# Kernel tuning notes

Hardware: AMD Instinct MI355X
Metric: run time of the kernel (lower is better)

## Reference

```python
import jax, jax.numpy as jnp
import numpy as np

NEG_SLOPE = 0.2


def gat_conv(x, src, dst, W, a_src, a_dst, bias, heads, out_ch):
    # x: [N, F_in]; src/dst: [E] (message flows src -> dst, softmax over dst)
    N = x.shape[0]
    h = (x @ W).reshape(N, heads, out_ch)              # [N, H, C]
    alpha_s = (h * a_src).sum(-1)                      # [N, H]
    alpha_d = (h * a_dst).sum(-1)                      # [N, H]
    e = jax.nn.leaky_relu(alpha_s[src] + alpha_d[dst], NEG_SLOPE)  # [E, H]
    # segment softmax over destination nodes (every node has a self loop)
    emax = jax.ops.segment_max(e, dst, num_segments=N)             # [N, H]
    ee = jnp.exp(e - emax[dst])
    denom = jax.ops.segment_sum(ee, dst, num_segments=N)           # [N, H]
    alpha = ee / denom[dst]                                        # [E, H]
    msg = h[src] * alpha[..., None]                                # [E, H, C]
    out = jax.ops.segment_sum(msg, dst, num_segments=N)            # [N, H, C]
    return out.reshape(N, heads * out_ch) + bias


def setup_inputs() -> dict:
    key = jax.random.key(0)
    ks = jax.random.split(key, 12)
    N, E, EL = 100000, 1600000, 100000
    F_in, C, H = 128, 64, 2
    glorot = lambda k, shp: jax.random.normal(k, shp, jnp.float32) * np.sqrt(2.0 / (shp[0] + shp[-1]))
    return {
        "x": jax.random.normal(ks[0], (N, F_in), jnp.float32),
        "edge_index": jax.random.randint(ks[1], (2, E), 0, N, jnp.int32),
        "edge_label_index": jax.random.randint(ks[2], (2, EL), 0, N, jnp.int32),
        "W1": glorot(ks[3], (F_in, H * C)),
        "a_src1": glorot(ks[4], (H, C)),
        "a_dst1": glorot(ks[5], (H, C)),
        "b1": jnp.zeros((H * C,), jnp.float32),
        "W2": glorot(ks[6], (H * C, C)),
        "a_src2": glorot(ks[7], (1, C)),
        "a_dst2": glorot(ks[8], (1, C)),
        "b2": jnp.zeros((C,), jnp.float32),
    }


def reference(x, edge_index, edge_label_index, W1, a_src1, a_dst1, b1, W2, a_src2, a_dst2, b2):
    N = x.shape[0]
    # add self loops (PyG GATConv default)
    loop = jnp.arange(N, dtype=edge_index.dtype)
    src = jnp.concatenate([edge_index[0], loop])
    dst = jnp.concatenate([edge_index[1], loop])
    H, C = a_src1.shape[0], a_src1.shape[1]
    z = jax.nn.elu(gat_conv(x, src, dst, W1, a_src1, a_dst1, b1, H, C))
    z = gat_conv(z, src, dst, W2, a_src2, a_dst2, b2, 1, C)         # [N, C]
    # decode: dot product of endpoint embeddings
    return (z[edge_label_index[0]] * z[edge_label_index[1]]).sum(axis=1)
```

## Files before the change

kernel.cpp:

```cpp
#include <hip/hip_runtime.h>
#include <hip/hip_bf16.h>

#define NEG_SLOPE 0.2f
#define LRELU(v) ((v) > 0.f ? (v) : NEG_SLOPE * (v))
#define BBITS 7
#define BSZ 128
#define BCAP 3072

typedef unsigned short ushort_t;
typedef unsigned int uint_t;
typedef float v2f __attribute__((ext_vector_type(2)));
typedef float f32x4 __attribute__((ext_vector_type(4)));
typedef short bf16x8 __attribute__((ext_vector_type(8)));

static inline int cdiv(int a, int b) { return (a + b - 1) / b; }

__device__ __forceinline__ float wsum(float v) {
#pragma unroll
    for (int o = 32; o; o >>= 1) v += __shfl_xor(v, o);
    return v;
}
__device__ __forceinline__ ushort_t f2bfbits(float f) {
    __hip_bfloat16 b = __float2bfloat16(f);
    return *reinterpret_cast<ushort_t*>(&b);
}

__global__ __launch_bounds__(256) void k_zero_int(int* p, int n) {
    int i = blockIdx.x * 256 + threadIdx.x;
    if (i < n) p[i] = 0;
}

__global__ __launch_bounds__(256) void k_bscatter(const int* __restrict__ ei, int E, int ET, int NB,
                                                  int* __restrict__ bcur,
                                                  uint_t* __restrict__ tmp) {
    extern __shared__ int sm2[];
    int* hist = sm2;
    int* cur = sm2 + NB;
    const int CH = 8192;
    int c0 = blockIdx.x * CH;
    int c1 = min(ET, c0 + CH);
    for (int i = threadIdx.x; i < NB; i += 256) hist[i] = 0;
    __syncthreads();
    for (int i = c0 + threadIdx.x; i < c1; i += 256) {
        int d = (i < E) ? ei[E + i] : (i - E);
        atomicAdd(&hist[d >> BBITS], 1);
    }
    __syncthreads();
    for (int i = threadIdx.x; i < NB; i += 256) {
        int c = hist[i];
        cur[i] = c ? atomicAdd(&bcur[i], c) : 0;
    }
    __syncthreads();
    for (int i = c0 + threadIdx.x; i < c1; i += 256) {
        int s = (i < E) ? ei[i] : (i - E);
        int d = (i < E) ? ei[E + i] : (i - E);
        int b = d >> BBITS;
        int pos = atomicAdd(&cur[b], 1);
        pos = min(pos, BCAP - 1);
        tmp[(size_t)b * BCAP + pos] = ((uint_t)(d & (BSZ - 1)) << 25) | (uint_t)s;
    }
}

__global__ void k_scan_small(const int* __restrict__ bcnt, int NB,
                             int* __restrict__ boff, int* __restrict__ offs, int N, int ET) {
    extern __shared__ int sm[];
    for (int i = threadIdx.x; i < NB; i += blockDim.x) sm[i] = bcnt[i];
    __syncthreads();
    if (threadIdx.x == 0) {
        int run = 0;
        for (int i = 0; i < NB; i++) { int c = sm[i]; sm[i] = run; run += c; }
    }
    __syncthreads();
    for (int i = threadIdx.x; i < NB; i += blockDim.x) boff[i] = sm[i];
    if (threadIdx.x == 0) { boff[NB] = ET; offs[N] = ET; }
}

__global__ __launch_bounds__(256) void k_csrfin(const uint_t* __restrict__ tmp,
                                                const int* __restrict__ boff, int NB, int N,
                                                int* __restrict__ offs, int* __restrict__ ssrc) {
    __shared__ int deg[BSZ], cur[BSZ], sc[BSZ];
    int b = blockIdx.x;
    int node0 = b << BBITS;
    int nn = min(BSZ, N - node0);
    int r0 = boff[b], r1 = boff[b + 1];
    int cnt = r1 - r0;
    const uint_t* tb = tmp + (size_t)b * BCAP;
    int t = threadIdx.x;
    if (t < BSZ) deg[t] = 0;
    __syncthreads();
    for (int j = t; j < cnt; j += 256) {
        int dloc = (int)(tb[j] >> 25);
        atomicAdd(&deg[dloc], 1);
    }
    __syncthreads();
    if (t < BSZ) sc[t] = deg[t];
    __syncthreads();
    for (int o = 1; o < BSZ; o <<= 1) {
        int v = 0;
        if (t < BSZ && t >= o) v = sc[t - o];
        __syncthreads();
        if (t < BSZ) sc[t] += v;
        __syncthreads();
    }
    if (t < BSZ) {
        int ex = sc[t] - deg[t];
        cur[t] = r0 + ex;
        if (t < nn) offs[node0 + t] = r0 + ex;
    }
    __syncthreads();
    for (int j = t; j < cnt; j += 256) {
        uint_t v = tb[j];
        int dloc = (int)(v >> 25);
        int s = (int)(v & 0x1FFFFFFu);
        int pos = atomicAdd(&cur[dloc], 1);
        ssrc[pos] = s;
    }
}

__global__ __launch_bounds__(256) void k_wt(const float* __restrict__ W1, ushort_t* __restrict__ Wt1,
                                            const float* __restrict__ W2, ushort_t* __restrict__ Wt2) {
    int idx = blockIdx.x * 256 + threadIdx.x;
    if (idx < 128 * 128) {
        int k = idx >> 7, n = idx & 127;
        Wt1[n * 128 + k] = f2bfbits(W1[idx]);
    } else if (idx < 128 * 128 + 128 * 64) {
        int j = idx - 128 * 128;
        int k = j >> 6, n = j & 63;
        Wt2[n * 128 + k] = f2bfbits(W2[j]);
    }
}

template <int M, int H, bool INBF16>
__global__ __launch_bounds__(256) void k_gemm_mfma(const void* __restrict__ xin,
                                                   const ushort_t* __restrict__ Wt,
                                                   const float* __restrict__ a_src,
                                                   const float* __restrict__ a_dst,
                                                   ushort_t* __restrict__ h,
                                                   float* __restrict__ as, float* __restrict__ ad,
                                                   int N) {
    constexpr int T = M / 16;
    int t = threadIdx.x;
    int w = t >> 6;
    int lane = t & 63;
    int ln = lane & 15;
    int q = lane >> 4;
    int rowA = blockIdx.x * 64 + w * 16 + ln;
    int rowD0 = blockIdx.x * 64 + w * 16 + q * 4;

    f32x4 acc[T];
#pragma unroll
    for (int i = 0; i < T; i++) acc[i] = (f32x4){0.f, 0.f, 0.f, 0.f};

#pragma unroll
    for (int kc = 0; kc < 4; kc++) {
        bf16x8 afrag;
        if (INBF16) {
            if (rowA < N)
                afrag = *(const bf16x8*)((const ushort_t*)xin + (size_t)rowA * 128 + kc * 32 + q * 8);
            else
#pragma unroll
                for (int j = 0; j < 8; j++) afrag[j] = 0;
        } else {
            float xv[8];
            if (rowA < N) {
                const float* xf = (const float*)xin;
                float4 v0 = *(const float4*)(xf + (size_t)rowA * 128 + kc * 32 + q * 8);
                float4 v1 = *(const float4*)(xf + (size_t)rowA * 128 + kc * 32 + q * 8 + 4);
                xv[0] = v0.x; xv[1] = v0.y; xv[2] = v0.z; xv[3] = v0.w;
                xv[4] = v1.x; xv[5] = v1.y; xv[6] = v1.z; xv[7] = v1.w;
            } else {
#pragma unroll
                for (int j = 0; j < 8; j++) xv[j] = 0.f;
            }
#pragma unroll
            for (int j = 0; j < 8; j++) afrag[j] = (short)f2bfbits(xv[j]);
        }
#pragma unroll
        for (int tt = 0; tt < T; tt++) {
            bf16x8 bfrag = *(const bf16x8*)(Wt + (size_t)(tt * 16 + ln) * 128 + kc * 32 + q * 8);
            acc[tt] = __builtin_amdgcn_mfma_f32_16x16x32_bf16(afrag, bfrag, acc[tt], 0, 0, 0);
        }
    }

#pragma unroll
    for (int tt = 0; tt < T; tt++)
#pragma unroll
        for (int r = 0; r < 4; r++) {
            int row = rowD0 + r;
            if (row < N) h[(size_t)row * M + tt * 16 + ln] = f2bfbits(acc[tt][r]);
        }

    float avs[T], avd[T];
#pragma unroll
    for (int tt = 0; tt < T; tt++) {
        avs[tt] = a_src[tt * 16 + ln];
        avd[tt] = a_dst[tt * 16 + ln];
    }
#pragma unroll
    for (int r = 0; r < 4; r++) {
        int row = rowD0 + r;
        if (H == 2) {
            float ps0 = 0.f, ps1 = 0.f, pd0 = 0.f, pd1 = 0.f;
#pragma unroll
            for (int tt = 0; tt < T / 2; tt++) { ps0 += acc[tt][r] * avs[tt]; pd0 += acc[tt][r] * avd[tt]; }
#pragma unroll
            for (int tt = T / 2; tt < T; tt++) { ps1 += acc[tt][r] * avs[tt]; pd1 += acc[tt][r] * avd[tt]; }
#pragma unroll
            for (int o = 8; o; o >>= 1) {
                ps0 += __shfl_down(ps0, o, 16); pd0 += __shfl_down(pd0, o, 16);
                ps1 += __shfl_down(ps1, o, 16); pd1 += __shfl_down(pd1, o, 16);
            }
            if (ln == 0 && row < N) {
                as[(size_t)row * 2] = ps0; as[(size_t)row * 2 + 1] = ps1;
                ad[(size_t)row * 2] = pd0; ad[(size_t)row * 2 + 1] = pd1;
            }
        } else {
            float ps = 0.f, pd = 0.f;
#pragma unroll
            for (int tt = 0; tt < T; tt++) { ps += acc[tt][r] * avs[tt]; pd += acc[tt][r] * avd[tt]; }
#pragma unroll
            for (int o = 8; o; o >>= 1) {
                ps += __shfl_down(ps, o, 16); pd += __shfl_down(pd, o, 16);
            }
            if (ln == 0 && row < N) { as[row] = ps; ad[row] = pd; }
        }
    }
}

template <int H, bool ELU_ACT, bool OUT_BF16>
__global__ __launch_bounds__(256) void k_agg_fused(const int* __restrict__ offs,
                                                   const int* __restrict__ ssrc,
                                                   const float* __restrict__ as,
                                                   const float* __restrict__ ad,
                                                   const ushort_t* __restrict__ h,
                                                   const float* __restrict__ bias,
                                                   void* __restrict__ z, int N) {
    constexpr int G = 16 * H;
    constexpr int EPW = 64 / G;
    constexpr int RB = H * 128;
    __shared__ __align__(16) uint2 lmeta[4][64 * H];
    int wv = threadIdx.x >> 6;
    int lane = threadIdx.x & 63;
    int d = (blockIdx.x * 256 + threadIdx.x) >> 6;
    if (d >= N) return;
    uint2* mw = lmeta[wv];
    int cpos = lane % G;
    int sub = lane / G;
    int hself = (H == 2) ? (cpos >> 4) : 0;
    const char* hb = (const char*)h;
    int cpo8 = cpos * 8;
    const char* mbase = (const char*)mw + ((H == 2) ? (sub * 16 + hself * 8) : (sub * 8));

    float adh0 = ad[(size_t)d * H];
    float adh1 = (H == 2) ? ad[(size_t)d * H + 1] : 0.f;
    float denp[2] = {0.f, 0.f};
    v2f acc2[2];
    acc2[0] = (v2f){0.f, 0.f};
    acc2[1] = (v2f){0.f, 0.f};

    int e0 = offs[d], e1 = offs[d + 1];
    for (int cb = e0; cb < e1; cb += 64) {
        int ne = min(64, e1 - cb);
        unsigned so = 0;
        float p0 = 0.f, p1 = 0.f;
        if (lane < ne) {
            int s_l = ssrc[cb + lane];
            so = (unsigned)s_l * RB;
            if (H == 2) {
                float2 av = ((const float2*)as)[s_l];
                p0 = __expf(LRELU(av.x + adh0));
                p1 = __expf(LRELU(av.y + adh1));
            } else {
                p0 = __expf(LRELU(as[s_l] + adh0));
            }
        }
        denp[0] += p0;
        denp[1] += p1;
        if (H == 2) {
            ((uint4*)mw)[lane] = make_uint4(so, __float_as_uint(p0), so, __float_as_uint(p1));
        } else {
            mw[lane] = make_uint2(so, __float_as_uint(p0));
        }
        int ng = (ne + EPW - 1) / EPW;
        for (int g0 = 0; g0 < ng; g0 += 4) {
            uint2 m[4];
#pragma unroll
            for (int g = 0; g < 4; g++) m[g] = *(const uint2*)(mbase + (g0 + g) * 32);
            uint2 hv[4];
#pragma unroll
            for (int g = 0; g < 4; g++) hv[g] = *(const uint2*)(hb + (m[g].x + cpo8));
#pragma unroll
            for (int g = 0; g < 4; g++) {
                float pvs = __uint_as_float(m[g].y);
                v2f pv = {pvs, pvs};
                v2f t0 = {__uint_as_float(hv[g].x << 16), __uint_as_float(hv[g].x & 0xffff0000u)};
                v2f t1 = {__uint_as_float(hv[g].y << 16), __uint_as_float(hv[g].y & 0xffff0000u)};
                acc2[0] += pv * t0;
                acc2[1] += pv * t1;
            }
        }
    }
#pragma unroll
    for (int o = G; o < 64; o <<= 1) {
        acc2[0][0] += __shfl_xor(acc2[0][0], o);
        acc2[0][1] += __shfl_xor(acc2[0][1], o);
        acc2[1][0] += __shfl_xor(acc2[1][0], o);
        acc2[1][1] += __shfl_xor(acc2[1][1], o);
    }
    float den0 = wsum(denp[0]);
    float den1 = (H == 2) ? wsum(denp[1]) : den0;
    if (lane < G) {
        float inv = 1.f / ((H == 2 && hself) ? den1 : den0);
        float vout[4];
        vout[0] = acc2[0][0] * inv + bias[cpos * 4 + 0];
        vout[1] = acc2[0][1] * inv + bias[cpos * 4 + 1];
        vout[2] = acc2[1][0] * inv + bias[cpos * 4 + 2];
        vout[3] = acc2[1][1] * inv + bias[cpos * 4 + 3];
        if (ELU_ACT) {
#pragma unroll
            for (int i = 0; i < 4; i++) vout[i] = vout[i] > 0.f ? vout[i] : expm1f(vout[i]);
        }
        if (OUT_BF16) {
            ushort4 pk;
            pk.x = f2bfbits(vout[0]); pk.y = f2bfbits(vout[1]);
            pk.z = f2bfbits(vout[2]); pk.w = f2bfbits(vout[3]);
            *(ushort4*)((ushort_t*)z + (size_t)d * (H * 64) + cpos * 4) = pk;
        } else {
            *(float4*)((float*)z + (size_t)d * (H * 64) + cpos * 4) =
                make_float4(vout[0], vout[1], vout[2], vout[3]);
        }
    }
}

__global__ __launch_bounds__(256) void k_decode(const int* __restrict__ eli,
                                                const float* __restrict__ z,
                                                float* __restrict__ out, int EL) {
    int wid = (blockIdx.x * 256 + threadIdx.x) >> 6;
    int lane = threadIdx.x & 63;
    int pi = wid * 4 + (lane >> 4);
    if (pi >= EL) return;
    int hl = lane & 15;
    int a = eli[pi], b = eli[EL + pi];
    float4 za = ((const float4*)(z + (size_t)a * 64))[hl];
    float4 zb = ((const float4*)(z + (size_t)b * 64))[hl];
    float p = za.x * zb.x + za.y * zb.y + za.z * zb.z + za.w * zb.w;
#pragma unroll
    for (int o = 8; o; o >>= 1) p += __shfl_down(p, o, 16);
    if (hl == 0) out[pi] = p;
}

extern "C" void kernel_launch(void* const* d_in, const int* in_sizes, int n_in,
                              void* d_out, int out_size, void* d_ws, size_t ws_size,
                              hipStream_t stream) {
    const float* x   = (const float*)d_in[0];
    const int*   ei  = (const int*)d_in[1];
    const int*   eli = (const int*)d_in[2];
    const float* W1  = (const float*)d_in[3];
    const float* as1 = (const float*)d_in[4];
    const float* ad1 = (const float*)d_in[5];
    const float* b1  = (const float*)d_in[6];
    const float* W2  = (const float*)d_in[7];
    const float* as2 = (const float*)d_in[8];
    const float* ad2 = (const float*)d_in[9];
    const float* b2  = (const float*)d_in[10];

    int N  = in_sizes[0] / 128;
    int E  = in_sizes[1] / 2;
    int EL = in_sizes[2] / 2;
    int ET = E + N;
    int NB = cdiv(N, BSZ);

    char* ws = (char*)d_ws;
    size_t off = 0;
    auto alloc = [&](size_t nbytes) -> void* {
        void* p = ws + off;
        off += (nbytes + 255) & ~(size_t)255;
        return p;
    };
    ushort_t* Hbuf = (ushort_t*)alloc((size_t)N * 128 * 2);
    char*     Zbuf = (char*)alloc((size_t)N * 128 * 2);
    float*    AS   = (float*)alloc((size_t)N * 2 * 4);
    float*    AD   = (float*)alloc((size_t)N * 2 * 4);
    int*      OFF  = (int*)alloc((size_t)(N + 1) * 4);
    int*      SSRC = (int*)alloc((size_t)ET * 4);
    int*      BOFF = (int*)alloc((size_t)(NB + 1) * 4);
    int*      BCUR = (int*)alloc((size_t)NB * 4);
    ushort_t* WT1  = (ushort_t*)alloc(128 * 128 * 2);
    ushort_t* WT2  = (ushort_t*)alloc(64 * 128 * 2);
    uint_t*   TMP  = (uint_t*)Zbuf;

    k_zero_int<<<cdiv(NB, 256), 256, 0, stream>>>(BCUR, NB);
    k_bscatter<<<cdiv(ET, 8192), 256, 2 * NB * 4, stream>>>(ei, E, ET, NB, BCUR, TMP);
    k_scan_small<<<1, 256, NB * 4, stream>>>(BCUR, NB, BOFF, OFF, N, ET);
    k_csrfin<<<NB, 256, 0, stream>>>(TMP, BOFF, NB, N, OFF, SSRC);

    k_wt<<<cdiv(128 * 128 + 128 * 64, 256), 256, 0, stream>>>(W1, WT1, W2, WT2);

    k_gemm_mfma<128, 2, false><<<cdiv(N, 64), 256, 0, stream>>>(x, WT1, as1, ad1, Hbuf, AS, AD, N);
    k_agg_fused<2, true, true><<<cdiv(N, 4), 256, 0, stream>>>(OFF, SSRC, AS, AD, Hbuf, b1, Zbuf, N);

    k_gemm_mfma<64, 1, true><<<cdiv(N, 64), 256, 0, stream>>>(Zbuf, WT2, as2, ad2, Hbuf, AS, AD, N);
    k_agg_fused<1, false, false><<<cdiv(N, 4), 256, 0, stream>>>(OFF, SSRC, AS, AD, Hbuf, b2, Zbuf, N);

    k_decode<<<cdiv(EL, 16), 256, 0, stream>>>(eli, (const float*)Zbuf, (float*)d_out, EL);
}
```

Baseline: 339.5 us.

## Merge init kernels, fold bucket scan into CSR finish, store final embeddings in bf16

Combines bucket-counter zeroing with the weight transpose/convert kernel and removes the single-threaded scan kernel by having each CSR-finish block reduce preceding bucket counts itself. The bucket scatter keeps destination indices in registers to avoid reloading them. The second layer output is now written in bf16 and the decoder reads bf16, halving its gather traffic. Fewer launches and less serial work are traded for redundant per-block reductions and reduced output precision.

```diff
diff --git a/kernel.cpp b/kernel.cpp
--- a/kernel.cpp
+++ b/kernel.cpp
@@ -25,9 +25,19 @@
     return *reinterpret_cast<ushort_t*>(&b);
 }
 
-__global__ __launch_bounds__(256) void k_zero_int(int* p, int n) {
-    int i = blockIdx.x * 256 + threadIdx.x;
-    if (i < n) p[i] = 0;
+__global__ __launch_bounds__(256) void k_init(int* __restrict__ bcur, int NB,
+                                              const float* __restrict__ W1, ushort_t* __restrict__ Wt1,
+                                              const float* __restrict__ W2, ushort_t* __restrict__ Wt2) {
+    int idx = blockIdx.x * 256 + threadIdx.x;
+    if (idx < NB) bcur[idx] = 0;
+    if (idx < 128 * 128) {
+        int k = idx >> 7, n = idx & 127;
+        Wt1[n * 128 + k] = f2bfbits(W1[idx]);
+    } else if (idx < 128 * 128 + 128 * 64) {
+        int j = idx - 128 * 128;
+        int k = j >> 6, n = j & 63;
+        Wt2[n * 128 + k] = f2bfbits(W2[j]);
+    }
 }
 
 __global__ __launch_bounds__(256) void k_bscatter(const int* __restrict__ ei, int E, int ET, int NB,
@@ -38,55 +48,59 @@
     int* cur = sm2 + NB;
     const int CH = 8192;
     int c0 = blockIdx.x * CH;
-    int c1 = min(ET, c0 + CH);
-    for (int i = threadIdx.x; i < NB; i += 256) hist[i] = 0;
-    __syncthreads();
-    for (int i = c0 + threadIdx.x; i < c1; i += 256) {
-        int d = (i < E) ? ei[E + i] : (i - E);
-        atomicAdd(&hist[d >> BBITS], 1);
-    }
-    __syncthreads();
-    for (int i = threadIdx.x; i < NB; i += 256) {
+    int t = threadIdx.x;
+    int dreg[32];
+    for (int i = t; i < NB; i += 256) hist[i] = 0;
+    __syncthreads();
+#pragma unroll
+    for (int j = 0; j < 32; j++) {
+        int i = c0 + j * 256 + t;
+        int d = -1;
+        if (i < ET) d = (i < E) ? ei[E + i] : (i - E);
+        dreg[j] = d;
+        if (d >= 0) atomicAdd(&hist[d >> BBITS], 1);
+    }
+    __syncthreads();
+    for (int i = t; i < NB; i += 256) {
         int c = hist[i];
         cur[i] = c ? atomicAdd(&bcur[i], c) : 0;
     }
     __syncthreads();
-    for (int i = c0 + threadIdx.x; i < c1; i += 256) {
-        int s = (i < E) ? ei[i] : (i - E);
-        int d = (i < E) ? ei[E + i] : (i - E);
-        int b = d >> BBITS;
-        int pos = atomicAdd(&cur[b], 1);
-        pos = min(pos, BCAP - 1);
-        tmp[(size_t)b * BCAP + pos] = ((uint_t)(d & (BSZ - 1)) << 25) | (uint_t)s;
-    }
-}
-
-__global__ void k_scan_small(const int* __restrict__ bcnt, int NB,
-                             int* __restrict__ boff, int* __restrict__ offs, int N, int ET) {
-    extern __shared__ int sm[];
-    for (int i = threadIdx.x; i < NB; i += blockDim.x) sm[i] = bcnt[i];
-    __syncthreads();
-    if (threadIdx.x == 0) {
-        int run = 0;
-        for (int i = 0; i < NB; i++) { int c = sm[i]; sm[i] = run; run += c; }
-    }
-    __syncthreads();
-    for (int i = threadIdx.x; i < NB; i += blockDim.x) boff[i] = sm[i];
-    if (threadIdx.x == 0) { boff[NB] = ET; offs[N] = ET; }
+#pragma unroll
+    for (int j = 0; j < 32; j++) {
+        int i = c0 + j * 256 + t;
+        int d = dreg[j];
+        if (d >= 0) {
+            int s = (i < E) ? ei[i] : (i - E);
+            int b = d >> BBITS;
+            int pos = atomicAdd(&cur[b], 1);
+            pos = min(pos, BCAP - 1);
+            tmp[(size_t)b * BCAP + pos] = ((uint_t)(d & (BSZ - 1)) << 25) | (uint_t)s;
+        }
+    }
 }
 
 __global__ __launch_bounds__(256) void k_csrfin(const uint_t* __restrict__ tmp,
-                                                const int* __restrict__ boff, int NB, int N,
+                                                const int* __restrict__ bcnt, int NB, int N, int ET,
                                                 int* __restrict__ offs, int* __restrict__ ssrc) {
-    __shared__ int deg[BSZ], cur[BSZ], sc[BSZ];
+    __shared__ int deg[BSZ], cur[BSZ], sc[BSZ], red[256];
     int b = blockIdx.x;
+    int t = threadIdx.x;
+    int part = 0;
+    for (int i = t; i < b; i += 256) part += bcnt[i];
+    red[t] = part;
+    __syncthreads();
+    for (int o = 128; o; o >>= 1) {
+        if (t < o) red[t] += red[t + o];
+        __syncthreads();
+    }
+    int r0 = red[0];
+    int cnt = min(bcnt[b], BCAP);
     int node0 = b << BBITS;
     int nn = min(BSZ, N - node0);
-    int r0 = boff[b], r1 = boff[b + 1];
-    int cnt = r1 - r0;
     const uint_t* tb = tmp + (size_t)b * BCAP;
-    int t = threadIdx.x;
     if (t < BSZ) deg[t] = 0;
+    if (b == 0 && t == 0) offs[N] = ET;
     __syncthreads();
     for (int j = t; j < cnt; j += 256) {
         int dloc = (int)(tb[j] >> 25);
@@ -114,19 +128,6 @@
         int s = (int)(v & 0x1FFFFFFu);
         int pos = atomicAdd(&cur[dloc], 1);
         ssrc[pos] = s;
-    }
-}
-
-__global__ __launch_bounds__(256) void k_wt(const float* __restrict__ W1, ushort_t* __restrict__ Wt1,
-                                            const float* __restrict__ W2, ushort_t* __restrict__ Wt2) {
-    int idx = blockIdx.x * 256 + threadIdx.x;
-    if (idx < 128 * 128) {
-        int k = idx >> 7, n = idx & 127;
-        Wt1[n * 128 + k] = f2bfbits(W1[idx]);
-    } else if (idx < 128 * 128 + 128 * 64) {
-        int j = idx - 128 * 128;
-        int k = j >> 6, n = j & 63;
-        Wt2[n * 128 + k] = f2bfbits(W2[j]);
     }
 }
 
@@ -333,7 +334,7 @@
 }
 
 __global__ __launch_bounds__(256) void k_decode(const int* __restrict__ eli,
-                                                const float* __restrict__ z,
+                                                const ushort_t* __restrict__ z,
                                                 float* __restrict__ out, int EL) {
     int wid = (blockIdx.x * 256 + threadIdx.x) >> 6;
     int lane = threadIdx.x & 63;
@@ -341,9 +342,12 @@
     if (pi >= EL) return;
     int hl = lane & 15;
     int a = eli[pi], b = eli[EL + pi];
-    float4 za = ((const float4*)(z + (size_t)a * 64))[hl];
-    float4 zb = ((const float4*)(z + (size_t)b * 64))[hl];
-    float p = za.x * zb.x + za.y * zb.y + za.z * zb.z + za.w * zb.w;
+    uint2 ua = *(const uint2*)(z + (size_t)a * 64 + hl * 4);
+    uint2 ub = *(const uint2*)(z + (size_t)b * 64 + hl * 4);
+    float p = __uint_as_float(ua.x << 16) * __uint_as_float(ub.x << 16) +
+              __uint_as_float(ua.x & 0xffff0000u) * __uint_as_float(ub.x & 0xffff0000u) +
+              __uint_as_float(ua.y << 16) * __uint_as_float(ub.y << 16) +
+              __uint_as_float(ua.y & 0xffff0000u) * __uint_as_float(ub.y & 0xffff0000u);
 #pragma unroll
     for (int o = 8; o; o >>= 1) p += __shfl_down(p, o, 16);
     if (hl == 0) out[pi] = p;
@@ -383,24 +387,20 @@
     float*    AD   = (float*)alloc((size_t)N * 2 * 4);
     int*      OFF  = (int*)alloc((size_t)(N + 1) * 4);
     int*      SSRC = (int*)alloc((size_t)ET * 4);
-    int*      BOFF = (int*)alloc((size_t)(NB + 1) * 4);
     int*      BCUR = (int*)alloc((size_t)NB * 4);
     ushort_t* WT1  = (ushort_t*)alloc(128 * 128 * 2);
     ushort_t* WT2  = (ushort_t*)alloc(64 * 128 * 2);
     uint_t*   TMP  = (uint_t*)Zbuf;
 
-    k_zero_int<<<cdiv(NB, 256), 256, 0, stream>>>(BCUR, NB);
+    k_init<<<cdiv(128 * 128 + 128 * 64, 256), 256, 0, stream>>>(BCUR, NB, W1, WT1, W2, WT2);
     k_bscatter<<<cdiv(ET, 8192), 256, 2 * NB * 4, stream>>>(ei, E, ET, NB, BCUR, TMP);
-    k_scan_small<<<1, 256, NB * 4, stream>>>(BCUR, NB, BOFF, OFF, N, ET);
-    k_csrfin<<<NB, 256, 0, stream>>>(TMP, BOFF, NB, N, OFF, SSRC);
-
-    k_wt<<<cdiv(128 * 128 + 128 * 64, 256), 256, 0, stream>>>(W1, WT1, W2, WT2);
+    k_csrfin<<<NB, 256, 0, stream>>>(TMP, BCUR, NB, N, ET, OFF, SSRC);
 
     k_gemm_mfma<128, 2, false><<<cdiv(N, 64), 256, 0, stream>>>(x, WT1, as1, ad1, Hbuf, AS, AD, N);
     k_agg_fused<2, true, true><<<cdiv(N, 4), 256, 0, stream>>>(OFF, SSRC, AS, AD, Hbuf, b1, Zbuf, N);
 
     k_gemm_mfma<64, 1, true><<<cdiv(N, 64), 256, 0, stream>>>(Zbuf, WT2, as2, ad2, Hbuf, AS, AD, N);
-    k_agg_fused<1, false, false><<<cdiv(N, 4), 256, 0, stream>>>(OFF, SSRC, AS, AD, Hbuf, b2, Zbuf, N);
-
-    k_decode<<<cdiv(EL, 16), 256, 0, stream>>>(eli, (const float*)Zbuf, (float*)d_out, EL);
-}
+    k_agg_fused<1, false, true><<<cdiv(N, 4), 256, 0, stream>>>(OFF, SSRC, AS, AD, Hbuf, b2, Zbuf, N);
+
+    k_decode<<<cdiv(EL, 16), 256, 0, stream>>>(eli, (const ushort_t*)Zbuf, (float*)d_out, EL);
+}
```

After: 324.1 us. 1.05x faster.
